# Kernel optimization log

Measured on AMD Instinct MI355X. Metric: run time of the kernel, lower is better.

Reference implementation:

```python
import jax, jax.numpy as jnp
import numpy as np

D, N, P, K = 128, 500000, 1024, 32


def setup_inputs() -> dict:
    key = jax.random.key(0)
    k1, k2, k3, k4 = jax.random.split(key, 4)
    U_base = jax.random.normal(k1, (D, N), dtype=jnp.float32)
    U = jax.random.normal(k2, (D, P), dtype=jnp.float32)
    # ragged partition: column j of U_base belongs to group seg_ids[j]
    merge_idx = jnp.arange(N, dtype=jnp.int64)
    seg_ids = jnp.sort(jax.random.randint(k3, (N,), 0, P)).astype(jnp.int64)
    # k nearest-neighbor indices per group for the Gram gather
    G = jax.random.randint(k4, (P, K), 0, P).astype(jnp.int64)
    return {"U_base": U_base, "U": U, "merge_idx": merge_idx,
            "seg_ids": seg_ids, "G": G}


def reference(U_base, U, merge_idx, seg_ids, G):
    # Flattened ragged loop: for each column j in group g = seg_ids[j],
    # dot(U[:, g], U_base[:, merge_idx[j]]); sum over dim 0 then square.
    dots = jnp.sum(U_base[:, merge_idx] * U[:, seg_ids], axis=0)  # [N]
    loss = -0.5 * jnp.sum(dots ** 2)
    # Gram-matrix neighbor gather: (U.T @ U)[G] -> [P, K, P]
    gram = U.T @ U  # [P, P]
    loss = loss - 0.5 * jnp.mean(gram[G] ** 2)
    return loss
```

## Files before the change

### kernel.cpp

```cpp
#include <hip/hip_runtime.h>

#define DIM 128
#define NCOLS 500000
#define PP 1024
#define KK 32
#define DCHUNK 32
#define NGROUPS (NCOLS / 4)
#define NB_DOTS ((NGROUPS + 63) / 64)
#define NB_GRAM 64
#define NB_K1 (1 + NB_GRAM + NB_DOTS)

typedef float floatx4 __attribute__((ext_vector_type(4)));


__global__ void __launch_bounds__(256) k1_kernel(
    const float* __restrict__ U_base, const float* __restrict__ U,
    const int* __restrict__ merge_idx, const int* __restrict__ seg_ids,
    const int* __restrict__ G, float* __restrict__ wsf) {
    const int bid = blockIdx.x;
    const int tid = threadIdx.x;

    if (bid >= 1 + NB_GRAM) {
        const int x = tid & 63, y = tid >> 6;
        const int tcol = (bid - 1 - NB_GRAM) * 64 + x;
        float a0 = 0.f, a1 = 0.f, a2 = 0.f, a3 = 0.f;
        if (tcol < NGROUPS) {
            int4 m = ((const int4*)merge_idx)[tcol];
            int4 g = ((const int4*)seg_ids)[tcol];
            const int d0 = y * DCHUNK;
            bool contig = (m.y == m.x + 1) & (m.z == m.x + 2) & (m.w == m.x + 3) & ((m.x & 3) == 0);
            bool sameg = (g.x == g.w);
            if (contig & sameg) {
                const float* ub = U_base + (size_t)d0 * NCOLS + m.x;
                const float* up = U + (size_t)d0 * PP + g.x;
                float ug[DCHUNK];
#pragma unroll
                for (int d = 0; d < DCHUNK; ++d) ug[d] = up[(size_t)d * PP];
#pragma unroll 8
                for (int d = 0; d < DCHUNK; ++d) {
                    floatx4 b = __builtin_nontemporal_load((const floatx4*)(ub + (size_t)d * NCOLS));
                    a0 += b.x * ug[d]; a1 += b.y * ug[d]; a2 += b.z * ug[d]; a3 += b.w * ug[d];
                }
            } else {
                for (int d = d0; d < d0 + DCHUNK; ++d) {
                    size_t rb = (size_t)d * NCOLS;
                    size_t ru = (size_t)d * PP;
                    a0 += U_base[rb + m.x] * U[ru + g.x];
                    a1 += U_base[rb + m.y] * U[ru + g.y];
                    a2 += U_base[rb + m.z] * U[ru + g.z];
                    a3 += U_base[rb + m.w] * U[ru + g.w];
                }
            }
        }
        __shared__ float4 red[256];
        red[y * 64 + x] = make_float4(a0, a1, a2, a3);
        __syncthreads();
        if (y == 0) {
            float s0 = 0.f, s1 = 0.f, s2 = 0.f, s3 = 0.f;
#pragma unroll
            for (int yy = 0; yy < 4; ++yy) {
                float4 r = red[yy * 64 + x];
                s0 += r.x; s1 += r.y; s2 += r.z; s3 += r.w;
            }
            float v = s0 * s0 + s1 * s1 + s2 * s2 + s3 * s3;
#pragma unroll
            for (int off = 32; off > 0; off >>= 1) v += __shfl_down(v, off, 64);
            if (x == 0) atomicAdd(&wsf[0], v);
        }
    } else if (bid == 0) {
        __shared__ int hc[PP];
        for (int i = tid; i < PP; i += 256) hc[i] = 0;
        if (tid == 0) { wsf[1] = 0.0f; ((int*)wsf)[2] = 0; }
        __syncthreads();
        for (int i = tid; i < (PP * KK) / 4; i += 256) {
            int4 gg = ((const int4*)G)[i];
            atomicAdd(&hc[gg.x], 1); atomicAdd(&hc[gg.y], 1);
            atomicAdd(&hc[gg.z], 1); atomicAdd(&hc[gg.w], 1);
        }
        __syncthreads();
        int* counts = (int*)(wsf + 4);
        for (int i = tid; i < PP; i += 256) counts[i] = hc[i];
    } else {
        float* M = wsf + 4 + PP;
        int t = (bid - 1) * 256 + tid;
        int d = t >> 7, e = t & 127;
        const float4* ud = (const float4*)(U + (size_t)d * PP);
        const float4* ue = (const float4*)(U + (size_t)e * PP);
        float acc = 0.0f;
#pragma unroll 4
        for (int p = 0; p < PP / 4; ++p) {
            float4 a = ud[p], b = ue[p];
            acc += a.x * b.x + a.y * b.y + a.z * b.z + a.w * b.w;
        }
        M[t] = acc;
    }
}

__global__ void __launch_bounds__(128) k2_kernel(
    const float* __restrict__ U, float* __restrict__ wsf, float* __restrict__ out) {
    __shared__ float u_s[DIM];
    __shared__ float red[DIM];
    const float* M = wsf + 4 + PP;
    const int* counts = (const int*)(wsf + 4);
    int r = blockIdx.x;
    int d = threadIdx.x;
    u_s[d] = U[(size_t)d * PP + r];
    __syncthreads();
    float t = 0.0f;
#pragma unroll 8
    for (int e = 0; e < DIM; ++e)
        t += M[e * DIM + d] * u_s[e];
    red[d] = u_s[d] * t;
    __syncthreads();
    for (int s = 64; s > 0; s >>= 1) {
        if (d < s) red[d] += red[d + s];
        __syncthreads();
    }
    if (d == 0) {
        atomicAdd(&wsf[1], red[0] * (float)counts[r]);
        __threadfence();
        int old = atomicAdd(((int*)wsf) + 2, 1);
        if (old == PP - 1) {
            float s1 = atomicAdd(&wsf[1], 0.0f);
            float s0 = wsf[0];
            out[0] = -0.5f * s0 - 0.5f * (s1 * (1.0f / 33554432.0f));
        }
    }
}

extern "C" void kernel_launch(void* const* d_in, const int* in_sizes, int n_in,
                              void* d_out, int out_size, void* d_ws, size_t ws_size,
                              hipStream_t stream) {
    const float* U_base  = (const float*)d_in[0];
    const float* U       = (const float*)d_in[1];
    const int* merge_idx = (const int*)d_in[2];
    const int* seg_ids   = (const int*)d_in[3];
    const int* G         = (const int*)d_in[4];
    float* out = (float*)d_out;
    float* wsf = (float*)d_ws;

    k1_kernel<<<NB_K1, 256, 0, stream>>>(U_base, U, merge_idx, seg_ids, G, wsf);
    k2_kernel<<<PP, DIM, 0, stream>>>(U, wsf, out);
}
```

Measured before the change: 404.6 us.

## Stage U group columns in LDS and give each thread all 128 dims

```diff
diff --git a/kernel.cpp b/kernel.cpp
--- a/kernel.cpp
+++ b/kernel.cpp
@@ -4,13 +4,13 @@
 #define NCOLS 500000
 #define PP 1024
 #define KK 32
-#define DCHUNK 32
 #define NGROUPS (NCOLS / 4)
-#define NB_DOTS ((NGROUPS + 63) / 64)
+#define GPB 256
+#define NB_DOTS ((NGROUPS + GPB - 1) / GPB)
 #define NB_GRAM 64
 #define NB_K1 (1 + NB_GRAM + NB_DOTS)
-
-typedef float floatx4 __attribute__((ext_vector_type(4)));
+#define TW 16
+#define PF 8
 
 
 __global__ void __launch_bounds__(256) k1_kernel(
@@ -21,52 +21,84 @@
     const int tid = threadIdx.x;
 
     if (bid >= 1 + NB_GRAM) {
-        const int x = tid & 63, y = tid >> 6;
-        const int tcol = (bid - 1 - NB_GRAM) * 64 + x;
+        __shared__ float tile[DIM * TW];
+        const int b = bid - 1 - NB_GRAM;
+        const int grp = b * GPB + tid;
+        const bool valid = (grp < NGROUPS);
+
+        const int c0 = b * GPB * 4;
+        const int clast = min(c0 + GPB * 4 - 1, NCOLS - 1);
+        const int gmin = seg_ids[c0];
+        const int gmax = seg_ids[clast];
+        const bool blk_fast = (gmax - gmin) < TW;
+
+        for (int i = tid; i < DIM * TW; i += 256) {
+            int d = i >> 4, c = i & (TW - 1);
+            int col = gmin + c;
+            tile[i] = (col < PP) ? U[(size_t)d * PP + col] : 0.0f;
+        }
+        __syncthreads();
+
+        int4 m = make_int4(0, 0, 0, 0), g = make_int4(0, 0, 0, 0);
+        bool fast = false;
+        if (valid) {
+            m = ((const int4*)merge_idx)[grp];
+            g = ((const int4*)seg_ids)[grp];
+            bool contig = (m.y == m.x + 1) & (m.z == m.x + 2) &
+                          (m.w == m.x + 3) & ((m.x & 3) == 0);
+            bool inr = (g.x >= gmin) & (g.x < gmin + TW) &
+                       (g.y >= gmin) & (g.y < gmin + TW) &
+                       (g.z >= gmin) & (g.z < gmin + TW) &
+                       (g.w >= gmin) & (g.w < gmin + TW);
+            fast = contig & blk_fast & inr;
+        }
+
         float a0 = 0.f, a1 = 0.f, a2 = 0.f, a3 = 0.f;
-        if (tcol < NGROUPS) {
-            int4 m = ((const int4*)merge_idx)[tcol];
-            int4 g = ((const int4*)seg_ids)[tcol];
-            const int d0 = y * DCHUNK;
-            bool contig = (m.y == m.x + 1) & (m.z == m.x + 2) & (m.w == m.x + 3) & ((m.x & 3) == 0);
-            bool sameg = (g.x == g.w);
-            if (contig & sameg) {
-                const float* ub = U_base + (size_t)d0 * NCOLS + m.x;
-                const float* up = U + (size_t)d0 * PP + g.x;
-                float ug[DCHUNK];
+
+        if (valid && !fast) {
+            for (int d = 0; d < DIM; ++d) {
+                const float* rb = U_base + (size_t)d * NCOLS;
+                const float* ru = U + (size_t)d * PP;
+                a0 += rb[m.x] * ru[g.x];
+                a1 += rb[m.y] * ru[g.y];
+                a2 += rb[m.z] * ru[g.z];
+                a3 += rb[m.w] * ru[g.w];
+            }
+        }
+        if (fast) {
+            const float* ub = U_base + m.x;
+            const int tx = g.x - gmin, ty = g.y - gmin;
+            const int tz = g.z - gmin, tw = g.w - gmin;
+            float4 buf[PF];
 #pragma unroll
-                for (int d = 0; d < DCHUNK; ++d) ug[d] = up[(size_t)d * PP];
-#pragma unroll 8
-                for (int d = 0; d < DCHUNK; ++d) {
-                    floatx4 b = __builtin_nontemporal_load((const floatx4*)(ub + (size_t)d * NCOLS));
-                    a0 += b.x * ug[d]; a1 += b.y * ug[d]; a2 += b.z * ug[d]; a3 += b.w * ug[d];
-                }
-            } else {
-                for (int d = d0; d < d0 + DCHUNK; ++d) {
-                    size_t rb = (size_t)d * NCOLS;
-                    size_t ru = (size_t)d * PP;
-                    a0 += U_base[rb + m.x] * U[ru + g.x];
-                    a1 += U_base[rb + m.y] * U[ru + g.y];
-                    a2 += U_base[rb + m.z] * U[ru + g.z];
-                    a3 += U_base[rb + m.w] * U[ru + g.w];
+            for (int k = 0; k < PF; ++k)
+                buf[k] = *(const float4*)(ub + (size_t)k * NCOLS);
+            for (int dd = 0; dd < DIM - PF; dd += PF) {
+#pragma unroll
+                for (int k = 0; k < PF; ++k) {
+                    float4 bv = buf[k];
+                    buf[k] = *(const float4*)(ub + (size_t)(dd + PF + k) * NCOLS);
+                    const int d = dd + k;
+                    a0 += bv.x * tile[d * TW + tx];
+                    a1 += bv.y * tile[d * TW + ty];
+                    a2 += bv.z * tile[d * TW + tz];
+                    a3 += bv.w * tile[d * TW + tw];
                 }
             }
+#pragma unroll
+            for (int k = 0; k < PF; ++k) {
+                const int d = DIM - PF + k;
+                float4 bv = buf[k];
+                a0 += bv.x * tile[d * TW + tx];
+                a1 += bv.y * tile[d * TW + ty];
+                a2 += bv.z * tile[d * TW + tz];
+                a3 += bv.w * tile[d * TW + tw];
+            }
         }
-        __shared__ float4 red[256];
-        red[y * 64 + x] = make_float4(a0, a1, a2, a3);
-        __syncthreads();
-        if (y == 0) {
-            float s0 = 0.f, s1 = 0.f, s2 = 0.f, s3 = 0.f;
+        float v = a0 * a0 + a1 * a1 + a2 * a2 + a3 * a3;
 #pragma unroll
-            for (int yy = 0; yy < 4; ++yy) {
-                float4 r = red[yy * 64 + x];
-                s0 += r.x; s1 += r.y; s2 += r.z; s3 += r.w;
-            }
-            float v = s0 * s0 + s1 * s1 + s2 * s2 + s3 * s3;
-#pragma unroll
-            for (int off = 32; off > 0; off >>= 1) v += __shfl_down(v, off, 64);
-            if (x == 0) atomicAdd(&wsf[0], v);
-        }
+        for (int off = 32; off > 0; off >>= 1) v += __shfl_down(v, off, 64);
+        if ((tid & 63) == 0) atomicAdd(&wsf[0], v);
     } else if (bid == 0) {
         __shared__ int hc[PP];
         for (int i = tid; i < PP; i += 256) hc[i] = 0;
```

Result: no change. 408.2 us (+0.9%).
